# Kernel optimization log

Hardware: AMD Instinct MI355X
Metric: run time of the kernel (lower is better)

Reference implementation:

```python
import jax, jax.numpy as jnp
import numpy as np

B, S, D, H = 2, 2048, 1024, 16
DK = D // H


def setup_inputs() -> dict:
    key = jax.random.key(0)
    ks = jax.random.split(key, 11)
    std = 1.0 / np.sqrt(D)
    inp = {
        "query": jax.random.normal(ks[0], (B, S, D), jnp.float32),
        "key": jax.random.normal(ks[1], (B, S, D), jnp.float32),
        "value": jax.random.normal(ks[2], (B, S, D), jnp.float32),
        # True = masked position (torch masked_fill semantics); causal mask
        "mask": jnp.triu(jnp.ones((1, 1, S, S), jnp.bool_), k=1),
        "Wq": jax.random.normal(ks[3], (D, D), jnp.float32) * std,
        "bq": jnp.zeros((D,), jnp.float32),
        "Wk": jax.random.normal(ks[4], (D, D), jnp.float32) * std,
        "bk": jnp.zeros((D,), jnp.float32),
        "Wv": jax.random.normal(ks[5], (D, D), jnp.float32) * std,
        "bv": jnp.zeros((D,), jnp.float32),
        "Wo": jax.random.normal(ks[6], (D, D), jnp.float32) * std,
        "bo": jnp.zeros((D,), jnp.float32),
    }
    return inp


def _split_heads(x):
    b, s, _ = x.shape
    return x.reshape(b, s, H, DK).transpose(0, 2, 1, 3)  # [b, H, s, dk]


def reference(query, key, value, mask, Wq, bq, Wk, bk, Wv, bv, Wo, bo):
    q = _split_heads(query @ Wq + bq)
    k = _split_heads(key @ Wk + bk)
    v = _split_heads(value @ Wv + bv)
    scale = 1.0 / (DK ** 0.5)
    logits = jnp.einsum("bhqd,bhkd->bhqk", q, k) * scale
    logits = jnp.where(mask, -1.0e9, logits)
    w = jax.nn.softmax(logits, axis=-1)
    att = jnp.einsum("bhqk,bhkd->bhqd", w, v)  # [B, H, S, dk]
    # NOTE: faithful to the original bug -- view() without permuting heads back,
    # i.e. a raw row-major reshape [B,H,S,dk] -> [B,S,H*dk].
    att = att.reshape(att.shape[0], att.shape[2], -1)
    out = att @ Wo + bo
    return out
```

## Files before the change

kernel.cpp:

```cpp
#include <hip/hip_runtime.h>
#include <hip/hip_bf16.h>

typedef __hip_bfloat16 bf16;
typedef __attribute__((ext_vector_type(8))) short bf16x8;
typedef __attribute__((ext_vector_type(4))) float f32x4;

constexpr int Bc  = 2;
constexpr int Sc  = 2048;
constexpr int Dc  = 1024;
constexpr int Hc  = 16;
constexpr int DKc = 64;

__device__ __forceinline__ float bfbits2f(unsigned short u) {
  return __uint_as_float(((unsigned)u) << 16);
}
__device__ __forceinline__ unsigned short f2bfbits(float x) {
  bf16 h = __float2bfloat16(x);
  return *reinterpret_cast<unsigned short*>(&h);
}
__device__ __forceinline__ void store1_dyn(char* base, size_t ei, int isf32, float v) {
  if (isf32) *reinterpret_cast<float*>(base + ei * 4) = v;
  else       *reinterpret_cast<bf16*>(base + ei * 2) = __float2bfloat16(v);
}
__device__ __forceinline__ float fast_exp2(float x) {
  return __builtin_amdgcn_exp2f(x);
}
__device__ __forceinline__ unsigned pkbf16(float a, float b) {
  __hip_bfloat162 h = __float22bfloat162_rn(make_float2(a, b));
  return *reinterpret_cast<unsigned*>(&h);
}
__device__ __forceinline__ uint4 pack8(const float4& a, const float4& b) {
  uint4 r;
  r.x = pkbf16(a.x, a.y);
  r.y = pkbf16(a.z, a.w);
  r.z = pkbf16(b.x, b.y);
  r.w = pkbf16(b.z, b.w);
  return r;
}
__device__ __forceinline__ void gld16(const void* g, void* l) {
  __builtin_amdgcn_global_load_lds(
      (const __attribute__((address_space(1))) unsigned int*)g,
      (__attribute__((address_space(3))) unsigned int*)l, 16, 0, 0);
}

__global__ __launch_bounds__(256)
void prep_all(const char* __restrict__ W0, const char* __restrict__ W1,
              const char* __restrict__ W2, const char* __restrict__ W3,
              unsigned short* __restrict__ Wt_all,
              const char* __restrict__ b0, const char* __restrict__ b1,
              const char* __restrict__ b2, const char* __restrict__ b3,
              unsigned short* __restrict__ bb_all,
              const char* __restrict__ A0, const char* __restrict__ A1,
              const char* __restrict__ A2, bf16* __restrict__ B0,
              bf16* __restrict__ B1, bf16* __restrict__ B2,
              int* __restrict__ flag_out) {
  __shared__ unsigned short T[64][72];
  __shared__ int cnt[256];
  const int id = blockIdx.x;
  const int tid = threadIdx.x;

  {
    const unsigned short* q = reinterpret_cast<const unsigned short*>(A0);
    int c = 0;
    for (int i = tid; i < 2048; i += 256) {
      const unsigned short u = q[i];
      const int e = (u >> 7) & 0xFF;
      if (e >= 134 || e <= 90) ++c;
    }
    cnt[tid] = c;
    __syncthreads();
    for (int s = 128; s > 0; s >>= 1) {
      if (tid < s) cnt[tid] += cnt[tid + s];
      __syncthreads();
    }
  }
  const int dyn = (cnt[0] > 64) ? 1 : 0;

  if (id < 1024) {
    const int z = id >> 8, rem = id & 255;
    const int n0 = (rem & 15) * 64, k0 = (rem >> 4) * 64;
    const char* W = (z == 0) ? W0 : (z == 1) ? W1 : (z == 2) ? W2 : W3;
    unsigned short* Wt = Wt_all + (size_t)z * Dc * Dc;
    const int r = tid >> 2, c16 = (tid & 3) * 16;

    unsigned short us[16];
    if (dyn) {
      const float4* p = reinterpret_cast<const float4*>(
          W + ((size_t)(k0 + r) * Dc + n0 + c16) * 4);
      const float4 f0 = p[0], f1 = p[1], f2 = p[2], f3 = p[3];
      const float fv[16] = {f0.x, f0.y, f0.z, f0.w, f1.x, f1.y, f1.z, f1.w,
                            f2.x, f2.y, f2.z, f2.w, f3.x, f3.y, f3.z, f3.w};
#pragma unroll
      for (int i = 0; i < 16; ++i) us[i] = f2bfbits(fv[i]);
    } else {
      const ushort4* p = reinterpret_cast<const ushort4*>(
          W + ((size_t)(k0 + r) * Dc + n0 + c16) * 2);
      const ushort4 u0 = p[0], u1 = p[1], u2 = p[2], u3 = p[3];
      us[0] = u0.x;  us[1] = u0.y;  us[2] = u0.z;  us[3] = u0.w;
      us[4] = u1.x;  us[5] = u1.y;  us[6] = u1.z;  us[7] = u1.w;
      us[8] = u2.x;  us[9] = u2.y;  us[10] = u2.z; us[11] = u2.w;
      us[12] = u3.x; us[13] = u3.y; us[14] = u3.z; us[15] = u3.w;
    }
#pragma unroll
    for (int i = 0; i < 16; ++i) T[r][c16 + i] = us[i];
    __syncthreads();

    unsigned vs[8];
#pragma unroll
    for (int i = 0; i < 8; ++i)
      vs[i] = (unsigned)T[c16 + 2 * i][r] | ((unsigned)T[c16 + 2 * i + 1][r] << 16);
    uint4* op = reinterpret_cast<uint4*>(Wt + (size_t)(n0 + r) * Dc + k0 + c16);
    op[0] = make_uint4(vs[0], vs[1], vs[2], vs[3]);
    op[1] = make_uint4(vs[4], vs[5], vs[6], vs[7]);
  } else if (id < 1028) {
    const int x = id - 1024;
    if (x == 0 && tid == 0) flag_out[0] = dyn;
    const char* src = (x == 0) ? b0 : (x == 1) ? b1 : (x == 2) ? b2 : b3;
    for (int i = tid; i < Dc; i += 256) {
      float v = dyn ? reinterpret_cast<const float*>(src)[i]
                    : bfbits2f(reinterpret_cast<const unsigned short*>(src)[i]);
      bb_all[x * Dc + i] = f2bfbits(v);
    }
  } else {
    const int j = id - 1028;
    const int z = j >> 9, x = j & 511;
    const char* src = (z == 0) ? A0 : (z == 1) ? A1 : A2;
    bf16* dst = (z == 0) ? B0 : (z == 1) ? B1 : B2;
    const size_t n = (size_t)4096 * Dc;
    const size_t stride = (size_t)512 * 256 * 8;
    for (size_t i = ((size_t)x * 256 + tid) * 8; i < n; i += stride) {
      uint4 u;
      if (dyn) {
        const float4* p = reinterpret_cast<const float4*>(src + i * 4);
        u = pack8(p[0], p[1]);
      } else {
        u = *reinterpret_cast<const uint4*>(src + i * 2);
      }
      *reinterpret_cast<uint4*>(dst + i) = u;
    }
  }
}

__global__ __launch_bounds__(256)
void qkv_gemm_async(const bf16* __restrict__ A0, const bf16* __restrict__ A1,
                    const bf16* __restrict__ A2,
                    const unsigned short* __restrict__ Wt_all,
                    const unsigned short* __restrict__ bias_all,
                    bf16* __restrict__ C0, bf16* __restrict__ C1,
                    bf16* __restrict__ C2) {
  constexpr int K = Dc, N = Dc;
  __shared__ __align__(16) unsigned short At[128 * 32];
  __shared__ __align__(16) unsigned short Bt[128 * 32];

  const int z = blockIdx.z;
  const bf16* A = (z == 0) ? A0 : (z == 1) ? A1 : A2;
  bf16* C = (z == 0) ? C0 : (z == 1) ? C1 : C2;
  const float scale = (z == 0) ? 0.18033688011112042f : 1.0f;
  const unsigned short* Wt = Wt_all + (size_t)z * Dc * Dc;
  const unsigned short* bias = bias_all + z * Dc;

  const int tid = threadIdx.x;
  const int m0 = blockIdx.x * 128, n0 = blockIdx.y * 128;
  const int w = tid >> 6, lane = tid & 63;
  const int lo16 = lane & 15, quad = lane >> 4;
  const int wm = (w >> 1) * 64, wn = (w & 1) * 64;

  unsigned short* ldsA = &At[w * 1024 + lane * 8];
  unsigned short* ldsB = &Bt[w * 1024 + lane * 8];
  const bf16* gA = A + (size_t)(m0 + w * 32 + (lane >> 2)) * K + (lane & 3) * 8;
  const unsigned short* gB = Wt + (size_t)(n0 + w * 32 + (lane >> 2)) * K + (lane & 3) * 8;

  f32x4 acc[4][4] = {};

  for (int k0 = 0; k0 < K; k0 += 32) {
    gld16(gA + k0, ldsA);
    gld16(gA + (size_t)16 * K + k0, ldsA + 512);
    gld16(gB + k0, ldsB);
    gld16(gB + (size_t)16 * K + k0, ldsB + 512);
    __syncthreads();

    bf16x8 afr[4], bfr[4];
#pragma unroll
    for (int mt = 0; mt < 4; ++mt)
      afr[mt] = *reinterpret_cast<const bf16x8*>(&At[(wm + mt * 16 + lo16) * 32 + quad * 8]);
#pragma unroll
    for (int nt = 0; nt < 4; ++nt)
      bfr[nt] = *reinterpret_cast<const bf16x8*>(&Bt[(wn + nt * 16 + lo16) * 32 + quad * 8]);
#pragma unroll
    for (int mt = 0; mt < 4; ++mt)
#pragma unroll
      for (int nt = 0; nt < 4; ++nt)
        acc[mt][nt] = __builtin_amdgcn_mfma_f32_16x16x32_bf16(afr[mt], bfr[nt],
                                                              acc[mt][nt], 0, 0, 0);
    __syncthreads();
  }

  float bv[4];
#pragma unroll
  for (int nt = 0; nt < 4; ++nt)
    bv[nt] = bfbits2f(bias[n0 + wn + nt * 16 + lo16]);
#pragma unroll
  for (int mt = 0; mt < 4; ++mt)
#pragma unroll
    for (int r = 0; r < 4; ++r) {
      const int row = m0 + wm + mt * 16 + quad * 4 + r;
#pragma unroll
      for (int nt = 0; nt < 4; ++nt) {
        const int col = n0 + wn + nt * 16 + lo16;
        C[(size_t)row * N + col] = __float2bfloat16((acc[mt][nt][r] + bv[nt]) * scale);
      }
    }
}

__global__ __launch_bounds__(256)
void qkv_gemm(const char* __restrict__ A0, const char* __restrict__ A1,
              const char* __restrict__ A2, const unsigned short* __restrict__ Wt_all,
              const unsigned short* __restrict__ bias_all,
              bf16* __restrict__ C0, bf16* __restrict__ C1, bf16* __restrict__ C2,
              const int* __restrict__ flagp) {
  constexpr int K = Dc, N = Dc;
  __shared__ __align__(16) unsigned short At[128][32];
  __shared__ __align__(16) unsigned short Bt[128][32];

  const int z = blockIdx.z;
  const char* A = (z == 0) ? A0 : (z == 1) ? A1 : A2;
  bf16* C = (z == 0) ? C0 : (z == 1) ? C1 : C2;
  const float scale = (z == 0) ? 0.18033688011112042f : 1.0f;
  const unsigned short* Wt = Wt_all + (size_t)z * Dc * Dc;
  const unsigned short* bias = bias_all + z * Dc;
  const int af = flagp[0];

  const int tid = threadIdx.x;
  const int m0 = blockIdx.x * 128, n0 = blockIdx.y * 128;
  const int w = tid >> 6, lane = tid & 63;
  const int lo16 = lane & 15, quad = lane >> 4;
  const int wm = (w >> 1) * 64, wn = (w & 1) * 64;
  const int sr = tid >> 1, sh = (tid & 1) * 16;

  f32x4 acc[4][4] = {};

  for (int k0 = 0; k0 < K; k0 += 32) {
    uint4 a_lo, a_hi;
    if (af) {
      const float4* p = reinterpret_cast<const float4*>(
          A + ((size_t)(m0 + sr) * K + k0 + sh) * 4);
      a_lo = pack8(p[0], p[1]);
      a_hi = pack8(p[2], p[3]);
    } else {
      const uint4* p = reinterpret_cast<const uint4*>(
          A + ((size_t)(m0 + sr) * K + k0 + sh) * 2);
      a_lo = p[0];
      a_hi = p[1];
    }
    const uint4* wp = reinterpret_cast<const uint4*>(Wt + (size_t)(n0 + sr) * K + k0 + sh);
    const uint4 b_lo = wp[0], b_hi = wp[1];

    __syncthreads();
    *reinterpret_cast<uint4*>(&At[sr][sh])     = a_lo;
    *reinterpret_cast<uint4*>(&At[sr][sh + 8]) = a_hi;
    *reinterpret_cast<uint4*>(&Bt[sr][sh])     = b_lo;
    *reinterpret_cast<uint4*>(&Bt[sr][sh + 8]) = b_hi;
    __syncthreads();

    bf16x8 afr[4], bfr[4];
#pragma unroll
    for (int mt = 0; mt < 4; ++mt)
      afr[mt] = *reinterpret_cast<const bf16x8*>(&At[wm + mt * 16 + lo16][quad * 8]);
#pragma unroll
    for (int nt = 0; nt < 4; ++nt)
      bfr[nt] = *reinterpret_cast<const bf16x8*>(&Bt[wn + nt * 16 + lo16][quad * 8]);
#pragma unroll
    for (int mt = 0; mt < 4; ++mt)
#pragma unroll
      for (int nt = 0; nt < 4; ++nt)
        acc[mt][nt] = __builtin_amdgcn_mfma_f32_16x16x32_bf16(afr[mt], bfr[nt],
                                                              acc[mt][nt], 0, 0, 0);
  }

  float bv[4];
#pragma unroll
  for (int nt = 0; nt < 4; ++nt)
    bv[nt] = bfbits2f(bias[n0 + wn + nt * 16 + lo16]);
#pragma unroll
  for (int mt = 0; mt < 4; ++mt)
#pragma unroll
    for (int r = 0; r < 4; ++r) {
      const int row = m0 + wm + mt * 16 + quad * 4 + r;
#pragma unroll
      for (int nt = 0; nt < 4; ++nt) {
        const int col = n0 + wn + nt * 16 + lo16;
        C[(size_t)row * N + col] = __float2bfloat16((acc[mt][nt][r] + bv[nt]) * scale);
      }
    }
}

__global__ __launch_bounds__(256)
void out_gemm_async(const bf16* __restrict__ A, const unsigned short* __restrict__ Wt,
                    const unsigned short* __restrict__ bias, char* __restrict__ C,
                    const int* __restrict__ flagp) {
  constexpr int K = Dc, N = Dc;
  __shared__ __align__(16) unsigned short At[128 * 32];
  __shared__ __align__(16) unsigned short Bt[128 * 32];

  const int cf = flagp[0];
  const int tid = threadIdx.x;
  const int m0 = blockIdx.x * 128, n0 = blockIdx.y * 128;
  const int w = tid >> 6, lane = tid & 63;
  const int lo16 = lane & 15, quad = lane >> 4;
  const int wm = (w >> 1) * 64, wn = (w & 1) * 64;

  unsigned short* ldsA = &At[w * 1024 + lane * 8];
  unsigned short* ldsB = &Bt[w * 1024 + lane * 8];
  const bf16* gA = A + (size_t)(m0 + w * 32 + (lane >> 2)) * K + (lane & 3) * 8;
  const unsigned short* gB = Wt + (size_t)(n0 + w * 32 + (lane >> 2)) * K + (lane & 3) * 8;

  f32x4 acc[4][4] = {};

  for (int k0 = 0; k0 < K; k0 += 32) {
    gld16(gA + k0, ldsA);
    gld16(gA + (size_t)16 * K + k0, ldsA + 512);
    gld16(gB + k0, ldsB);
    gld16(gB + (size_t)16 * K + k0, ldsB + 512);
    __syncthreads();

    bf16x8 afr[4], bfr[4];
#pragma unroll
    for (int mt = 0; mt < 4; ++mt)
      afr[mt] = *reinterpret_cast<const bf16x8*>(&At[(wm + mt * 16 + lo16) * 32 + quad * 8]);
#pragma unroll
    for (int nt = 0; nt < 4; ++nt)
      bfr[nt] = *reinterpret_cast<const bf16x8*>(&Bt[(wn + nt * 16 + lo16) * 32 + quad * 8]);
#pragma unroll
    for (int mt = 0; mt < 4; ++mt)
#pragma unroll
      for (int nt = 0; nt < 4; ++nt)
        acc[mt][nt] = __builtin_amdgcn_mfma_f32_16x16x32_bf16(afr[mt], bfr[nt],
                                                              acc[mt][nt], 0, 0, 0);
    __syncthreads();
  }

  float bv[4];
#pragma unroll
  for (int nt = 0; nt < 4; ++nt)
    bv[nt] = bfbits2f(bias[n0 + wn + nt * 16 + lo16]);
#pragma unroll
  for (int mt = 0; mt < 4; ++mt)
#pragma unroll
    for (int r = 0; r < 4; ++r) {
      const int row = m0 + wm + mt * 16 + quad * 4 + r;
#pragma unroll
      for (int nt = 0; nt < 4; ++nt) {
        const int col = n0 + wn + nt * 16 + lo16;
        store1_dyn(C, (size_t)row * N + col, cf, acc[mt][nt][r] + bv[nt]);
      }
    }
}

__global__ __launch_bounds__(256, 2)
void attn_mfma(const bf16* __restrict__ Q, const bf16* __restrict__ K,
               const bf16* __restrict__ V, bf16* __restrict__ O) {
  __shared__ __align__(16) unsigned short Kt[64][72];
  __shared__ __align__(16) unsigned short Vt[64][72];
  __shared__ __align__(16) unsigned short St[4][32][72];
  __shared__ float Li[4][32];

  const int hb = blockIdx.x & 31;
  const int i  = blockIdx.x >> 5;
  const int g = i >> 3, r0 = i & 7;
  const int c = g ? (15 - r0) : r0;
  const int b = hb >> 4, h = hb & 15;
  const int q0 = c * 128;
  const int tid = threadIdx.x;
  const int w = tid >> 6;
  const int lane = tid & 63;
  const int lo16 = lane & 15, quad = lane >> 4;
  const size_t hd = (size_t)h * DKc;

  const int kr = tid >> 2, kc = (tid & 3) * 16;
  const int vk = (tid & 31) * 2, vd0 = (tid >> 5) * 8;

  const bf16* qrowA = Q + ((size_t)(b * Sc + q0 + w * 32 + lo16)) * Dc + hd;
  const bf16x8 qa0 = *reinterpret_cast<const bf16x8*>(qrowA + quad * 8);
  const bf16x8 qa1 = *reinterpret_cast<const bf16x8*>(qrowA + 32 + quad * 8);
  const bf16* qrowB = qrowA + (size_t)16 * Dc;
  const bf16x8 qb0 = *reinterpret_cast<const bf16x8*>(qrowB + quad * 8);
  const bf16x8 qb1 = *reinterpret_cast<const bf16x8*>(qrowB + 32 + quad * 8);

  f32x4 oA[4] = {f32x4{0,0,0,0}, f32x4{0,0,0,0}, f32x4{0,0,0,0}, f32x4{0,0,0,0}};
  f32x4 oB[4] = {f32x4{0,0,0,0}, f32x4{0,0,0,0}, f32x4{0,0,0,0}, f32x4{0,0,0,0}};
  float lsA = 0.f, lsB = 0.f;
  const int qgA = q0 + w * 32 + lo16;
  const int qgB = qgA + 16;
  const int qmaxA = q0 + w * 32 + 15;
  const int qmaxB = qmaxA + 16;
  const int nt = 2 * (c + 1);

  const bf16* ksrc = K + ((size_t)(b * Sc + kr)) * Dc + hd + kc;
  const bf16* vsrc = V + ((size_t)(b * Sc + vk)) * Dc + hd + vd0;

  uint4 rKa = *reinterpret_cast<const uint4*>(ksrc);
  uint4 rKb = *reinterpret_cast<const uint4*>(ksrc + 8);
  uint4 rVa = *reinterpret_cast<const uint4*>(vsrc);
  uint4 rVb = *reinterpret_cast<const uint4*>(vsrc + Dc);

  for (int t = 0; t < nt; ++t) {
    const int kt = t * 64;
    __syncthreads();
    *reinterpret_cast<uint4*>(&Kt[kr][kc])     = rKa;
    *reinterpret_cast<uint4*>(&Kt[kr][kc + 8]) = rKb;
    *reinterpret_cast<unsigned*>(&Vt[vd0 + 0][vk]) = (rVa.x & 0xffffu) | (rVb.x << 16);
    *reinterpret_cast<unsigned*>(&Vt[vd0 + 1][vk]) = (rVa.x >> 16)     | (rVb.x & 0xffff0000u);
    *reinterpret_cast<unsigned*>(&Vt[vd0 + 2][vk]) = (rVa.y & 0xffffu) | (rVb.y << 16);
    *reinterpret_cast<unsigned*>(&Vt[vd0 + 3][vk]) = (rVa.y >> 16)     | (rVb.y & 0xffff0000u);
    *reinterpret_cast<unsigned*>(&Vt[vd0 + 4][vk]) = (rVa.z & 0xffffu) | (rVb.z << 16);
    *reinterpret_cast<unsigned*>(&Vt[vd0 + 5][vk]) = (rVa.z >> 16)     | (rVb.z & 0xffff0000u);
    *reinterpret_cast<unsigned*>(&Vt[vd0 + 6][vk]) = (rVa.w & 0xffffu) | (rVb.w << 16);
    *reinterpret_cast<unsigned*>(&Vt[vd0 + 7][vk]) = (rVa.w >> 16)     | (rVb.w & 0xffff0000u);
    __syncthreads();

    if (t + 1 < nt) {
      const size_t off = (size_t)(t + 1) * 64 * Dc;
      rKa = *reinterpret_cast<const uint4*>(ksrc + off);
      rKb = *reinterpret_cast<const uint4*>(ksrc + off + 8);
      rVa = *reinterpret_cast<const uint4*>(vsrc + off);
      rVb = *reinterpret_cast<const uint4*>(vsrc + off + Dc);
    }

    if (kt > qmaxB) continue;
    const bool liveA = (kt <= qmaxA);

    bf16x8 ka[4], kb[4];
#pragma unroll
    for (int ct = 0; ct < 4; ++ct) {
      ka[ct] = *reinterpret_cast<const bf16x8*>(&Kt[ct * 16 + lo16][quad * 8]);
      kb[ct] = *reinterpret_cast<const bf16x8*>(&Kt[ct * 16 + lo16][32 + quad * 8]);
    }

    f32x4 sA[4] = {f32x4{0,0,0,0}, f32x4{0,0,0,0}, f32x4{0,0,0,0}, f32x4{0,0,0,0}};
    f32x4 sB[4] = {f32x4{0,0,0,0}, f32x4{0,0,0,0}, f32x4{0,0,0,0}, f32x4{0,0,0,0}};
    __builtin_amdgcn_s_setprio(1);
#pragma unroll
    for (int ct = 0; ct < 4; ++ct) {
      sB[ct] = __builtin_amdgcn_mfma_f32_16x16x32_bf16(ka[ct], qb0, sB[ct], 0, 0, 0);
      sB[ct] = __builtin_amdgcn_mfma_f32_16x16x32_bf16(kb[ct], qb1, sB[ct], 0, 0, 0);
    }
    if (liveA) {
#pragma unroll
      for (int ct = 0; ct < 4; ++ct) {
        sA[ct] = __builtin_amdgcn_mfma_f32_16x16x32_bf16(ka[ct], qa0, sA[ct], 0, 0, 0);
        sA[ct] = __builtin_amdgcn_mfma_f32_16x16x32_bf16(kb[ct], qa1, sA[ct], 0, 0, 0);
      }
    }
    __builtin_amdgcn_s_setprio(0);

    if (kt + 63 > q0 + w * 32 + 16) {
#pragma unroll
      for (int ct = 0; ct < 4; ++ct)
#pragma unroll
        for (int r = 0; r < 4; ++r)
          if (kt + ct * 16 + quad * 4 + r > qgB) sB[ct][r] = -1e9f;
    }
    if (liveA && (kt + 63 > q0 + w * 32)) {
#pragma unroll
      for (int ct = 0; ct < 4; ++ct)
#pragma unroll
        for (int r = 0; r < 4; ++r)
          if (kt + ct * 16 + quad * 4 + r > qgA) sA[ct][r] = -1e9f;
    }

#pragma unroll
    for (int ct = 0; ct < 4; ++ct) {
      const float p0 = fast_exp2(sB[ct][0]);
      const float p1 = fast_exp2(sB[ct][1]);
      const float p2 = fast_exp2(sB[ct][2]);
      const float p3 = fast_exp2(sB[ct][3]);
      lsB += (p0 + p1) + (p2 + p3);
      uint2 pk;
      pk.x = pkbf16(p0, p1);
      pk.y = pkbf16(p2, p3);
      *reinterpret_cast<uint2*>(&St[w][16 + lo16][ct * 16 + quad * 4]) = pk;
    }
    if (liveA) {
#pragma unroll
      for (int ct = 0; ct < 4; ++ct) {
        const float p0 = fast_exp2(sA[ct][0]);
        const float p1 = fast_exp2(sA[ct][1]);
        const float p2 = fast_exp2(sA[ct][2]);
        const float p3 = fast_exp2(sA[ct][3]);
        lsA += (p0 + p1) + (p2 + p3);
        uint2 pk;
        pk.x = pkbf16(p0, p1);
        pk.y = pkbf16(p2, p3);
        *reinterpret_cast<uint2*>(&St[w][lo16][ct * 16 + quad * 4]) = pk;
      }
    }

    const bf16x8 pb0 = *reinterpret_cast<const bf16x8*>(&St[w][16 + lo16][quad * 8]);
    const bf16x8 pb1 = *reinterpret_cast<const bf16x8*>(&St[w][16 + lo16][32 + quad * 8]);
    const bf16x8 pa0 = *reinterpret_cast<const bf16x8*>(&St[w][lo16][quad * 8]);
    const bf16x8 pa1 = *reinterpret_cast<const bf16x8*>(&St[w][lo16][32 + quad * 8]);
    __builtin_amdgcn_s_setprio(1);
#pragma unroll
    for (int ct = 0; ct < 4; ++ct) {
      const bf16x8 vb0 = *reinterpret_cast<const bf16x8*>(&Vt[ct * 16 + lo16][quad * 8]);
      const bf16x8 vb1 = *reinterpret_cast<const bf16x8*>(&Vt[ct * 16 + lo16][32 + quad * 8]);
      oB[ct] = __builtin_amdgcn_mfma_f32_16x16x32_bf16(pb0, vb0, oB[ct], 0, 0, 0);
      oB[ct] = __builtin_amdgcn_mfma_f32_16x16x32_bf16(pb1, vb1, oB[ct], 0, 0, 0);
      if (liveA) {
        oA[ct] = __builtin_amdgcn_mfma_f32_16x16x32_bf16(pa0, vb0, oA[ct], 0, 0, 0);
        oA[ct] = __builtin_amdgcn_mfma_f32_16x16x32_bf16(pa1, vb1, oA[ct], 0, 0, 0);
      }
    }
    __builtin_amdgcn_s_setprio(0);
  }

  lsA += __shfl_xor(lsA, 16);
  lsA += __shfl_xor(lsA, 32);
  lsB += __shfl_xor(lsB, 16);
  lsB += __shfl_xor(lsB, 32);
  if (quad == 0) {
    Li[w][lo16] = 1.f / lsA;
    Li[w][16 + lo16] = 1.f / lsB;
  }
  __builtin_amdgcn_wave_barrier();
  const f32x4 invA = *reinterpret_cast<const f32x4*>(&Li[w][quad * 4]);
  const f32x4 invB = *reinterpret_cast<const f32x4*>(&Li[w][16 + quad * 4]);

#pragma unroll
  for (int r = 0; r < 4; ++r) {
    bf16* opA = O + (((size_t)(b * Hc + h) * Sc) + q0 + w * 32 + quad * 4 + r) * DKc + lo16;
    bf16* opB = opA + (size_t)16 * DKc;
#pragma unroll
    for (int ct = 0; ct < 4; ++ct) {
      opA[ct * 16] = __float2bfloat16(oA[ct][r] * invA[r]);
      opB[ct * 16] = __float2bfloat16(oB[ct][r] * invB[r]);
    }
  }
}

extern "C" void kernel_launch(void* const* d_in, const int* in_sizes, int n_in,
                              void* d_out, int out_size, void* d_ws, size_t ws_size,
                              hipStream_t stream) {
  (void)in_sizes; (void)out_size;
  const char* query = (const char*)d_in[0];
  const char* key_  = (const char*)d_in[1];
  const char* value = (const char*)d_in[2];
  const int wb = n_in - 8;
  const char* Wq = (const char*)d_in[wb + 0];
  const char* bq = (const char*)d_in[wb + 1];
  const char* Wk = (const char*)d_in[wb + 2];
  const char* bk = (const char*)d_in[wb + 3];
  const char* Wv = (const char*)d_in[wb + 4];
  const char* bv = (const char*)d_in[wb + 5];
  const char* Wo = (const char*)d_in[wb + 6];
  const char* bo = (const char*)d_in[wb + 7];

  char* ws = (char*)d_ws;
  bf16* Qs  = (bf16*)(ws);
  bf16* Ks  = (bf16*)(ws + ((size_t)8  << 20));
  bf16* Vs  = (bf16*)(ws + ((size_t)16 << 20));
  bf16* att = (bf16*)(ws + ((size_t)24 << 20));
  unsigned short* Wt_all = (unsigned short*)(ws + ((size_t)32 << 20));
  unsigned short* bb_all = (unsigned short*)(ws + ((size_t)40 << 20));
  int* flag = (int*)(ws + ((size_t)40 << 20) + 16384);
  bf16* Qb = (bf16*)(ws + ((size_t)42 << 20));
  bf16* Kb = (bf16*)(ws + ((size_t)50 << 20));
  bf16* Vb = (bf16*)(ws + ((size_t)58 << 20));
  const bool big_ws = ws_size >= ((size_t)66 << 20);

  if (big_ws) {
    prep_all<<<2564, 256, 0, stream>>>(Wq, Wk, Wv, Wo, Wt_all, bq, bk, bv, bo,
                                       bb_all, query, key_, value, Qb, Kb, Vb, flag);
    qkv_gemm_async<<<dim3(32, 8, 3), 256, 0, stream>>>(Qb, Kb, Vb, Wt_all, bb_all,
                                                       Qs, Ks, Vs);
  } else {
    prep_all<<<1028, 256, 0, stream>>>(Wq, Wk, Wv, Wo, Wt_all, bq, bk, bv, bo,
                                       bb_all, query, key_, value,
                                       (bf16*)att, (bf16*)att, (bf16*)att, flag);
    qkv_gemm<<<dim3(32, 8, 3), 256, 0, stream>>>(query, key_, value, Wt_all, bb_all,
                                                 Qs, Ks, Vs, flag);
  }

  attn_mfma<<<dim3(512), 256, 0, stream>>>(Qs, Ks, Vs, att);

  out_gemm_async<<<dim3(32, 8), 256, 0, stream>>>(att, Wt_all + (size_t)3 * Dc * Dc,
                                                  bb_all + 3 * Dc, (char*)d_out, flag);
}
```

Before: 232.4 us.

## Split long causal query tiles across two blocks and merge partial results

The attention kernel gains a split-KV mode. Query tiles in the upper half of the sequence are each processed by two blocks over disjoint key ranges, giving 768 blocks with more even work instead of 512 with a long causal tail. Each split block writes unnormalized fp32 partial outputs and row sums to workspace, and a new merge kernel adds them and normalizes to bf16. This costs an extra launch and about 16 MB of fp32 partial traffic. It relies on no running-max rescaling, so summing raw partials is consistent with the existing softmax scheme.

Result: faster. 226.6 us (-2.5%).

```diff
diff --git a/kernel.cpp b/kernel.cpp
--- a/kernel.cpp
+++ b/kernel.cpp
@@ -356,18 +356,27 @@
     }
 }
 
+template <int SPLIT>
 __global__ __launch_bounds__(256, 2)
 void attn_mfma(const bf16* __restrict__ Q, const bf16* __restrict__ K,
-               const bf16* __restrict__ V, bf16* __restrict__ O) {
+               const bf16* __restrict__ V, bf16* __restrict__ O,
+               float* __restrict__ P, float* __restrict__ Lp) {
   __shared__ __align__(16) unsigned short Kt[64][72];
   __shared__ __align__(16) unsigned short Vt[64][72];
   __shared__ __align__(16) unsigned short St[4][32][72];
   __shared__ float Li[4][32];
 
   const int hb = blockIdx.x & 31;
-  const int i  = blockIdx.x >> 5;
-  const int g = i >> 3, r0 = i & 7;
-  const int c = g ? (15 - r0) : r0;
+  int c, t0, t1, part;
+  if constexpr (SPLIT) {
+    const int u = blockIdx.x >> 5;
+    if (u < 8)       { c = u;      t0 = 0;     t1 = 2 * c + 2; part = 0; }
+    else if (u < 16) { c = 23 - u; t0 = 0;     t1 = c + 1;     part = 1; }
+    else             { c = 31 - u; t0 = c + 1; t1 = 2 * c + 2; part = 2; }
+  } else {
+    const int i = blockIdx.x >> 5, g = i >> 3, r0 = i & 7;
+    c = g ? (15 - r0) : r0; t0 = 0; t1 = 2 * (c + 1); part = 0;
+  }
   const int b = hb >> 4, h = hb & 15;
   const int q0 = c * 128;
   const int tid = threadIdx.x;
@@ -393,17 +402,17 @@
   const int qgB = qgA + 16;
   const int qmaxA = q0 + w * 32 + 15;
   const int qmaxB = qmaxA + 16;
-  const int nt = 2 * (c + 1);
 
   const bf16* ksrc = K + ((size_t)(b * Sc + kr)) * Dc + hd + kc;
   const bf16* vsrc = V + ((size_t)(b * Sc + vk)) * Dc + hd + vd0;
 
-  uint4 rKa = *reinterpret_cast<const uint4*>(ksrc);
-  uint4 rKb = *reinterpret_cast<const uint4*>(ksrc + 8);
-  uint4 rVa = *reinterpret_cast<const uint4*>(vsrc);
-  uint4 rVb = *reinterpret_cast<const uint4*>(vsrc + Dc);
-
-  for (int t = 0; t < nt; ++t) {
+  const size_t off0 = (size_t)t0 * 64 * Dc;
+  uint4 rKa = *reinterpret_cast<const uint4*>(ksrc + off0);
+  uint4 rKb = *reinterpret_cast<const uint4*>(ksrc + off0 + 8);
+  uint4 rVa = *reinterpret_cast<const uint4*>(vsrc + off0);
+  uint4 rVb = *reinterpret_cast<const uint4*>(vsrc + off0 + Dc);
+
+  for (int t = t0; t < t1; ++t) {
     const int kt = t * 64;
     __syncthreads();
     *reinterpret_cast<uint4*>(&Kt[kr][kc])     = rKa;
@@ -418,7 +427,7 @@
     *reinterpret_cast<unsigned*>(&Vt[vd0 + 7][vk]) = (rVa.w >> 16)     | (rVb.w & 0xffff0000u);
     __syncthreads();
 
-    if (t + 1 < nt) {
+    if (t + 1 < t1) {
       const size_t off = (size_t)(t + 1) * 64 * Dc;
       rKa = *reinterpret_cast<const uint4*>(ksrc + off);
       rKb = *reinterpret_cast<const uint4*>(ksrc + off + 8);
@@ -518,6 +527,28 @@
   lsA += __shfl_xor(lsA, 32);
   lsB += __shfl_xor(lsB, 16);
   lsB += __shfl_xor(lsB, 32);
+
+  if (SPLIT && part != 0) {
+    float* Pp = P + ((size_t)(part - 1) * 32 + hb) * (size_t)(1024 * 64);
+    float* Lq = Lp + ((size_t)(part - 1) * 32 + hb) * 1024;
+    const int qlA = q0 - 1024 + w * 32;
+    if (quad == 0) {
+      Lq[qlA + lo16] = lsA;
+      Lq[qlA + 16 + lo16] = lsB;
+    }
+#pragma unroll
+    for (int r = 0; r < 4; ++r) {
+      float* pA = Pp + (size_t)(qlA + quad * 4 + r) * 64 + lo16;
+      float* pB = Pp + (size_t)(qlA + 16 + quad * 4 + r) * 64 + lo16;
+#pragma unroll
+      for (int ct = 0; ct < 4; ++ct) {
+        pA[ct * 16] = oA[ct][r];
+        pB[ct * 16] = oB[ct][r];
+      }
+    }
+    return;
+  }
+
   if (quad == 0) {
     Li[w][lo16] = 1.f / lsA;
     Li[w][16 + lo16] = 1.f / lsB;
@@ -536,6 +567,23 @@
       opB[ct * 16] = __float2bfloat16(oB[ct][r] * invB[r]);
     }
   }
+}
+
+__global__ __launch_bounds__(256)
+void merge_att(const float* __restrict__ P, const float* __restrict__ Lp,
+               bf16* __restrict__ att) {
+  const int e = blockIdx.x * 256 + threadIdx.x;
+  const int d4 = (e & 15) * 4;
+  const int q  = (e >> 4) & 1023;
+  const int hb = e >> 14;
+  const size_t pi = ((size_t)hb * 1024 + q) * 64 + d4;
+  const float4 a = *reinterpret_cast<const float4*>(P + pi);
+  const float4 c = *reinterpret_cast<const float4*>(P + (size_t)2097152 + pi);
+  const float inv = 1.f / (Lp[hb * 1024 + q] + Lp[32768 + hb * 1024 + q]);
+  uint2 o;
+  o.x = pkbf16((a.x + c.x) * inv, (a.y + c.y) * inv);
+  o.y = pkbf16((a.z + c.z) * inv, (a.w + c.w) * inv);
+  *reinterpret_cast<uint2*>(att + ((size_t)hb * 2048 + 1024 + q) * 64 + d4) = o;
 }
 
 extern "C" void kernel_launch(void* const* d_in, const int* in_sizes, int n_in,
@@ -566,6 +614,8 @@
   bf16* Qb = (bf16*)(ws + ((size_t)42 << 20));
   bf16* Kb = (bf16*)(ws + ((size_t)50 << 20));
   bf16* Vb = (bf16*)(ws + ((size_t)58 << 20));
+  float* Pw = (float*)(ws + ((size_t)42 << 20));
+  float* Lw = (float*)(ws + ((size_t)59 << 20));
   const bool big_ws = ws_size >= ((size_t)66 << 20);
 
   if (big_ws) {
@@ -573,15 +623,16 @@
                                        bb_all, query, key_, value, Qb, Kb, Vb, flag);
     qkv_gemm_async<<<dim3(32, 8, 3), 256, 0, stream>>>(Qb, Kb, Vb, Wt_all, bb_all,
                                                        Qs, Ks, Vs);
+    attn_mfma<1><<<dim3(768), 256, 0, stream>>>(Qs, Ks, Vs, att, Pw, Lw);
+    merge_att<<<dim3(2048), 256, 0, stream>>>(Pw, Lw, att);
   } else {
     prep_all<<<1028, 256, 0, stream>>>(Wq, Wk, Wv, Wo, Wt_all, bq, bk, bv, bo,
                                        bb_all, query, key_, value,
                                        (bf16*)att, (bf16*)att, (bf16*)att, flag);
     qkv_gemm<<<dim3(32, 8, 3), 256, 0, stream>>>(query, key_, value, Wt_all, bb_all,
                                                  Qs, Ks, Vs, flag);
-  }
-
-  attn_mfma<<<dim3(512), 256, 0, stream>>>(Qs, Ks, Vs, att);
+    attn_mfma<0><<<dim3(512), 256, 0, stream>>>(Qs, Ks, Vs, att, Pw, Lw);
+  }
 
   out_gemm_async<<<dim3(32, 8), 256, 0, stream>>>(att, Wt_all + (size_t)3 * Dc * Dc,
                                                   bb_all + 3 * Dc, (char*)d_out, flag);
```
